# Kernel tuning notes

Measured on AMD Instinct MI355X. Metric: run time of the kernel, lower is better.

Reference implementation:

```python
import jax, jax.numpy as jnp
import numpy as np

H = 8       # num_heads
HD = 32     # transformer_head_dim
LN_EPS = 1e-5


def _layernorm(x, g, b):
    m = jnp.mean(x, axis=-1, keepdims=True)
    v = jnp.mean(jnp.square(x - m), axis=-1, keepdims=True)
    return (x - m) * jax.lax.rsqrt(v + LN_EPS) * g + b


def setup_inputs() -> dict:
    key = jax.random.key(0)
    ks = jax.random.split(key, 8)
    D, DFF = 256, 1024
    B, N = 8, 2048
    s = 0.02  # weight init scale
    return {
        "x": jax.random.normal(ks[0], (B, N, D), jnp.float32),
        "w_qkv": jax.random.normal(ks[1], (3 * H * HD, D), jnp.float32) * s,
        "w_out": jax.random.normal(ks[2], (D, H * HD), jnp.float32) * s,
        "b_out": jnp.zeros((D,), jnp.float32),
        "w1": jax.random.normal(ks[3], (DFF, D), jnp.float32) * s,
        "wv": jax.random.normal(ks[4], (DFF, D), jnp.float32) * s,
        "w2": jax.random.normal(ks[5], (D, DFF), jnp.float32) * s,
        "ln1_g": jnp.ones((D,), jnp.float32),
        "ln1_b": jnp.zeros((D,), jnp.float32),
        "ln2_g": jnp.ones((D,), jnp.float32),
        "ln2_b": jnp.zeros((D,), jnp.float32),
    }


def reference(x, w_qkv, w_out, b_out, w1, wv, w2, ln1_g, ln1_b, ln2_g, ln2_b):
    B, N, D = x.shape
    scale = HD ** (-0.5)
    # --- MultiHeadedAttention ---
    qkv = x @ w_qkv.T                                   # [B,N,3*H*HD]
    q, k, v = jnp.split(qkv, 3, axis=-1)
    def to_heads(t):
        return t.reshape(B, N, H, HD).transpose(0, 2, 1, 3)  # [B,H,N,HD]
    q, k, v = to_heads(q), to_heads(k), to_heads(v)
    sim = jnp.einsum("bhid,bhjd->bhij", q, k) * scale   # [B,H,N,N]
    attn = jax.nn.softmax(sim, axis=-1)
    o = jnp.einsum("bhij,bhjd->bhid", attn, v)
    o = o.transpose(0, 2, 1, 3).reshape(B, N, H * HD)
    y = o @ w_out.T + b_out                             # attn output
    # --- attn AddNorm: ln(dropout(y)+x), dropout off ---
    x1 = _layernorm(y + x, ln1_g, ln1_b)
    # --- GEGLU FFN applied to y (faithful to source) ---
    ff = jax.nn.gelu(y @ w1.T, approximate=False) * (y @ wv.T)
    ff = ff @ w2.T
    # --- ff AddNorm ---
    return _layernorm(ff + x1, ln2_g, ln2_b)
```

## Files before the change

### kernel.cpp

```cpp
#include <hip/hip_runtime.h>

typedef unsigned short u16;
typedef __bf16 bf16;
typedef __bf16 bf16x8 __attribute__((ext_vector_type(8)));
typedef float f32x4 __attribute__((ext_vector_type(4)));
typedef unsigned short u16x8 __attribute__((ext_vector_type(8)));
typedef unsigned short u16x4 __attribute__((ext_vector_type(4)));
typedef unsigned short u16x2 __attribute__((ext_vector_type(2)));

#define DEVI static __device__ __forceinline__

DEVI float bf2f(u16 h) { return __builtin_bit_cast(float, (unsigned)h << 16); }
DEVI u16 cvt_bf(float f) { return __builtin_bit_cast(u16, (bf16)f); }

DEVI void gload16(const u16* g, u16* l) {
  __builtin_amdgcn_global_load_lds(
      (const __attribute__((address_space(1))) void*)g,
      (__attribute__((address_space(3))) void*)l, 16, 0, 0);
}

DEVI float gelu_exact(float x) {
  return 0.5f * x * (1.0f + erff(x * 0.70710678118654752f));
}

__global__ __launch_bounds__(256) void k_cast(const float* __restrict__ x,
                                              const float* __restrict__ wqkv,
                                              const float* __restrict__ wout,
                                              const float* __restrict__ w1,
                                              const float* __restrict__ wv,
                                              const float* __restrict__ w2,
                                              u16* __restrict__ dst0) {
  long i = (long)blockIdx.x * 256 + threadIdx.x;
  const float* src;
  u16* dst;
  long off;
  if (i < 1048576)       { src = x;    dst = dst0;           off = i; }
  else if (i < 1097728)  { src = wqkv; dst = dst0 + 4194304; off = i - 1048576; }
  else if (i < 1114112)  { src = wout; dst = dst0 + 4390912; off = i - 1097728; }
  else if (i < 1179648)  { src = w1;   dst = dst0 + 4456448; off = i - 1114112; }
  else if (i < 1245184)  { src = wv;   dst = dst0 + 4718592; off = i - 1179648; }
  else                   { src = w2;   dst = dst0 + 4980736; off = i - 1245184; }
  float4 f = reinterpret_cast<const float4*>(src)[off];
  u16x4 o;
  o[0] = cvt_bf(f.x); o[1] = cvt_bf(f.y); o[2] = cvt_bf(f.z); o[3] = cvt_bf(f.w);
  reinterpret_cast<u16x4*>(dst)[off] = o;
}

template <int BM, int BN, int NI>
__global__ __launch_bounds__(256) void k_gemm(const u16* __restrict__ A, const u16* __restrict__ B0,
                                              const u16* __restrict__ B1, int Nsplit,
                                              const float* __restrict__ bias,
                                              u16* __restrict__ C, int N, int K) {
  constexpr int MI = BM / 32;
  __shared__ u16 Alds[BM * 64];
  __shared__ u16 Blds[BN * 64];
  const int m0 = blockIdx.x * BM;
  const int n0 = blockIdx.y * BN;
  const u16* Ap = A + (long)m0 * K;
  const u16* Bp = (n0 < Nsplit) ? (B0 + (long)n0 * K) : (B1 + (long)(n0 - Nsplit) * K);
  const int tid = threadIdx.x, lane = tid & 63, wave = tid >> 6;
  const int wr = (wave >> 1) * (BM / 2), wc = (wave & 1) * (BN / 2);
  const int lr = lane & 15, g = lane >> 4;
  const int sr = lane >> 3, sg = lane & 7;

  f32x4 acc[MI][NI] = {};
  const int nk = K >> 6;
  for (int kt = 0; kt < nk; ++kt) {
    const int kb = kt << 6;
    __syncthreads();
#pragma unroll
    for (int c = 0; c < BM / 32; ++c) {
      const int row = wave * (BM / 4) + c * 8 + sr;
      gload16(Ap + (long)row * K + kb + ((sg ^ (row & 7)) << 3),
              &Alds[(wave * (BM / 4) + c * 8) << 6]);
    }
#pragma unroll
    for (int c = 0; c < BN / 32; ++c) {
      const int row = wave * (BN / 4) + c * 8 + sr;
      gload16(Bp + (long)row * K + kb + ((sg ^ ((row / NI) & 7)) << 3),
              &Blds[(wave * (BN / 4) + c * 8) << 6]);
    }
    __syncthreads();
#pragma unroll
    for (int kk = 0; kk < 2; ++kk) {
      bf16x8 av[MI], bv[NI];
#pragma unroll
      for (int i = 0; i < MI; ++i) {
        const int ra = wr + i * 16 + lr;
        av[i] = *reinterpret_cast<const bf16x8*>(&Alds[(ra << 6) + (((kk * 4 + g) ^ (ra & 7)) << 3)]);
      }
#pragma unroll
      for (int ni = 0; ni < NI; ++ni) {
        const int rb = wc + lr * NI + ni;
        bv[ni] = *reinterpret_cast<const bf16x8*>(&Blds[(rb << 6) + (((kk * 4 + g) ^ ((rb / NI) & 7)) << 3)]);
      }
#pragma unroll
      for (int mi = 0; mi < MI; ++mi)
#pragma unroll
        for (int ni = 0; ni < NI; ++ni)
          acc[mi][ni] = __builtin_amdgcn_mfma_f32_16x16x32_bf16(av[mi], bv[ni], acc[mi][ni], 0, 0, 0);
    }
  }
  const int colb = n0 + wc + lr * NI;
  float bvv[NI];
#pragma unroll
  for (int ni = 0; ni < NI; ++ni) bvv[ni] = bias ? bias[colb + ni] : 0.0f;
#pragma unroll
  for (int mi = 0; mi < MI; ++mi) {
#pragma unroll
    for (int r = 0; r < 4; ++r) {
      const long row = m0 + wr + mi * 16 + g * 4 + r;
      if constexpr (NI == 4) {
        u16x4 v;
#pragma unroll
        for (int ni = 0; ni < 4; ++ni) v[ni] = cvt_bf(acc[mi][ni][r] + bvv[ni]);
        *reinterpret_cast<u16x4*>(C + row * N + colb) = v;
      } else {
        u16x2 v;
#pragma unroll
        for (int ni = 0; ni < 2; ++ni) v[ni] = cvt_bf(acc[mi][ni][r] + bvv[ni]);
        *reinterpret_cast<u16x2*>(C + row * N + colb) = v;
      }
    }
  }
}

__global__ __launch_bounds__(256) void k_glu(const u16* __restrict__ A, const u16* __restrict__ W1,
                                             const u16* __restrict__ Wv, u16* __restrict__ C) {
  constexpr int K = 256, N = 1024;
  __shared__ u16 Alds[128 * 64];
  __shared__ u16 Blds[64 * 64];
  const int m0 = blockIdx.x * 128;
  const int n0h = blockIdx.y * 32;
  const u16* Ap = A + (long)m0 * K;
  const int tid = threadIdx.x, lane = tid & 63, wave = tid >> 6;
  const int lr = lane & 15, g = lane >> 4;
  const int sr = lane >> 3, sg = lane & 7;

  f32x4 acc[2][4] = {};
  for (int kt = 0; kt < 4; ++kt) {
    const int kb = kt << 6;
    __syncthreads();
#pragma unroll
    for (int c = 0; c < 4; ++c) {
      const int row = wave * 32 + c * 8 + sr;
      gload16(Ap + (long)row * K + kb + ((sg ^ (row & 7)) << 3), &Alds[(wave * 32 + c * 8) << 6]);
    }
#pragma unroll
    for (int c = 0; c < 2; ++c) {
      const int row = wave * 16 + c * 8 + sr;
      const u16* bp = (row & 1) ? Wv : W1;
      gload16(bp + (long)(n0h + (row >> 1)) * K + kb + ((sg ^ ((row >> 2) & 7)) << 3),
              &Blds[(wave * 16 + c * 8) << 6]);
    }
    __syncthreads();
#pragma unroll
    for (int kk = 0; kk < 2; ++kk) {
      bf16x8 av[2], bv[4];
#pragma unroll
      for (int i = 0; i < 2; ++i) {
        const int ra = wave * 32 + i * 16 + lr;
        av[i] = *reinterpret_cast<const bf16x8*>(&Alds[(ra << 6) + (((kk * 4 + g) ^ (ra & 7)) << 3)]);
      }
#pragma unroll
      for (int ni = 0; ni < 4; ++ni) {
        const int rb = lr * 4 + ni;
        bv[ni] = *reinterpret_cast<const bf16x8*>(&Blds[(rb << 6) + (((kk * 4 + g) ^ ((rb >> 2) & 7)) << 3)]);
      }
#pragma unroll
      for (int mi = 0; mi < 2; ++mi)
#pragma unroll
        for (int ni = 0; ni < 4; ++ni)
          acc[mi][ni] = __builtin_amdgcn_mfma_f32_16x16x32_bf16(av[mi], bv[ni], acc[mi][ni], 0, 0, 0);
    }
  }
  const int j0 = n0h + lr * 2;
#pragma unroll
  for (int mi = 0; mi < 2; ++mi) {
#pragma unroll
    for (int r = 0; r < 4; ++r) {
      const long row = m0 + wave * 32 + mi * 16 + g * 4 + r;
      u16x2 v;
      v[0] = cvt_bf(gelu_exact(acc[mi][0][r]) * acc[mi][1][r]);
      v[1] = cvt_bf(gelu_exact(acc[mi][2][r]) * acc[mi][3][r]);
      *reinterpret_cast<u16x2*>(C + row * N + j0) = v;
    }
  }
}

__global__ __launch_bounds__(256) void k_vt(const u16* __restrict__ qkv, u16* __restrict__ vt) {
  const int bh = blockIdx.x & 63, nt = blockIdx.x >> 6;
  const int b = bh >> 3, h = bh & 7;
  const int wave = threadIdx.x >> 6, lane = threadIdx.x & 63;
  const int dcol = wave * 8;
#pragma unroll
  for (int i = 0; i < 4; ++i) {
    const int nn = nt * 256 + i * 64 + lane;
    u16x8 v = *reinterpret_cast<const u16x8*>(qkv + (long)(b * 2048 + nn) * 768 + 512 + h * 32 + dcol);
#pragma unroll
    for (int j = 0; j < 8; ++j)
      vt[(long)(bh * 32 + dcol + j) * 2048 + nn] = v[j];
  }
}

__global__ __launch_bounds__(512) void k_attn(const u16* __restrict__ qkv, const u16* __restrict__ vt,
                                              u16* __restrict__ o) {
  __shared__ u16 Klds[2 * 4096];
  __shared__ u16 Vlds[2 * 4096];
  __shared__ u16 Plds[8 * 1024];
  const int id = blockIdx.x;
  const int qt = id >> 6, bh = id & 63;
  const int b = bh >> 3, h = bh & 7;
  const int tid = threadIdx.x, wave = tid >> 6, lane = tid & 63;
  const int lq = lane & 15, g = lane >> 4, lqh = lq & 7;

  const long qrow = (long)(b * 2048 + qt * 128 + wave * 16 + lq);
  u16x8 qraw = *reinterpret_cast<const u16x8*>(qkv + qrow * 768 + h * 32 + g * 8);
  bf16x8 qf;
#pragma unroll
  for (int j = 0; j < 8; ++j) qf[j] = (bf16)(bf2f(qraw[j]) * 0.25503486f);

  const int rK = tid >> 3, gpK = tid & 7, lK = gpK ^ (rK & 7);
  const u16* ksrc = qkv + (long)(b * 2048 + (lK >> 2) * 64 + rK) * 768 + 256 + h * 32 + (lK & 3) * 8;
  const int dV = tid >> 4, gpV = tid & 15, lV = (gpV & 8) | ((gpV & 7) ^ (dV & 7));
  const u16* vsrc = vt + (long)(bh * 32 + dV) * 2048 + lV * 8;
  u16* kdst = Klds + wave * 512;
  u16* vdst = Vlds + wave * 512;

  gload16(ksrc, kdst);
  gload16(vsrc, vdst);

  float m = -1e30f, l = 0.0f;
  f32x4 oacc[2] = {};
  const f32x4 zero = {0.0f, 0.0f, 0.0f, 0.0f};
  u16* Pw = Plds + wave * 1024;

  for (int kt = 0; kt < 16; ++kt) {
    const int bo = (kt & 1) * 4096;
    __syncthreads();
    if (kt + 1 < 16) {
      const int nbo = ((kt + 1) & 1) * 4096;
      gload16(ksrc + (long)(kt + 1) * 98304, kdst + nbo);
      gload16(vsrc + (kt + 1) * 128, vdst + nbo);
    }
    f32x4 s[8];
#pragma unroll
    for (int f = 0; f < 8; ++f) {
      const bf16x8 kf = *reinterpret_cast<const bf16x8*>(
          &Klds[bo + (((f & 3) * 16 + lq) << 6) + ((((f >> 2) * 4 + g) ^ lqh) << 3)]);
      s[f] = __builtin_amdgcn_mfma_f32_16x16x32_bf16(kf, qf, zero, 0, 0, 0);
    }
    float tmax = -1e30f;
#pragma unroll
    for (int f = 0; f < 8; ++f)
#pragma unroll
      for (int r = 0; r < 4; ++r) tmax = fmaxf(tmax, s[f][r]);
    tmax = fmaxf(tmax, __shfl_xor(tmax, 16));
    tmax = fmaxf(tmax, __shfl_xor(tmax, 32));
    const float mnew = fmaxf(m, tmax);
    const float alpha = exp2f(m - mnew);
    float rsum = 0.0f;
#pragma unroll
    for (int f = 0; f < 8; ++f)
#pragma unroll
      for (int r = 0; r < 4; ++r) {
        const float p = exp2f(s[f][r] - mnew);
        s[f][r] = p;
        rsum += p;
      }
    rsum += __shfl_xor(rsum, 16);
    rsum += __shfl_xor(rsum, 32);
    l = l * alpha + rsum;
    m = mnew;
#pragma unroll
    for (int di = 0; di < 2; ++di)
#pragma unroll
      for (int r = 0; r < 4; ++r) oacc[di][r] *= alpha;

#pragma unroll
    for (int pass = 0; pass < 2; ++pass) {
#pragma unroll
      for (int fi = 0; fi < 4; ++fi) {
        const int f = pass * 4 + fi;
        u16x4 pk;
#pragma unroll
        for (int r = 0; r < 4; ++r) pk[r] = cvt_bf(s[f][r]);
        *reinterpret_cast<u16x4*>(
            &Pw[(lq << 6) + (((fi * 2 + (g >> 1)) ^ lqh) << 3) + ((g & 1) << 2)]) = pk;
      }
#pragma unroll
      for (int ks2 = 0; ks2 < 2; ++ks2) {
        const bf16x8 pf = *reinterpret_cast<const bf16x8*>(
            &Pw[(lq << 6) + (((ks2 * 4 + g) ^ lqh) << 3)]);
        const int gl = (pass * 2 + ks2) * 4 + g;
        const int gp = (gl & 8) | ((gl & 7) ^ lqh);
#pragma unroll
        for (int di = 0; di < 2; ++di) {
          const bf16x8 vf = *reinterpret_cast<const bf16x8*>(
              &Vlds[bo + (((di * 16 + lq)) << 7) + (gp << 3)]);
          oacc[di] = __builtin_amdgcn_mfma_f32_16x16x32_bf16(vf, pf, oacc[di], 0, 0, 0);
        }
      }
    }
  }

  const float inv = 1.0f / l;
  const long orow = (long)(b * 2048 + qt * 128 + wave * 16 + lq);
#pragma unroll
  for (int di = 0; di < 2; ++di) {
    u16x4 ov;
#pragma unroll
    for (int r = 0; r < 4; ++r) ov[r] = cvt_bf(oacc[di][r] * inv);
    *reinterpret_cast<u16x4*>(o + orow * 256 + h * 32 + di * 16 + g * 4) = ov;
  }
}

__global__ __launch_bounds__(256) void k_ln(const u16* __restrict__ yin, const float* __restrict__ xres,
                                            const float* __restrict__ gw, const float* __restrict__ bw,
                                            float* __restrict__ out) {
  const int row = blockIdx.x * 4 + (threadIdx.x >> 6);
  const int lane = threadIdx.x & 63;
  const long base = (long)row * 256 + lane * 4;
  const float4 xv = *reinterpret_cast<const float4*>(xres + base);
  const u16x4 yv = *reinterpret_cast<const u16x4*>(yin + base);
  float s0 = bf2f(yv[0]) + xv.x;
  float s1 = bf2f(yv[1]) + xv.y;
  float s2 = bf2f(yv[2]) + xv.z;
  float s3 = bf2f(yv[3]) + xv.w;
  float sum = s0 + s1 + s2 + s3;
  float sq = s0 * s0 + s1 * s1 + s2 * s2 + s3 * s3;
#pragma unroll
  for (int msk = 1; msk < 64; msk <<= 1) {
    sum += __shfl_xor(sum, msk);
    sq += __shfl_xor(sq, msk);
  }
  const float mean = sum * (1.0f / 256.0f);
  const float var = sq * (1.0f / 256.0f) - mean * mean;
  const float rstd = rsqrtf(var + 1e-5f);
  const int c = lane * 4;
  float4 ov;
  ov.x = (s0 - mean) * rstd * gw[c + 0] + bw[c + 0];
  ov.y = (s1 - mean) * rstd * gw[c + 1] + bw[c + 1];
  ov.z = (s2 - mean) * rstd * gw[c + 2] + bw[c + 2];
  ov.w = (s3 - mean) * rstd * gw[c + 3] + bw[c + 3];
  *reinterpret_cast<float4*>(out + base) = ov;
}

extern "C" void kernel_launch(void* const* d_in, const int* in_sizes, int n_in,
                              void* d_out, int out_size, void* d_ws, size_t ws_size,
                              hipStream_t stream) {
  (void)in_sizes; (void)n_in; (void)out_size;
  if (ws_size < 136314880ULL) return;

  const float* x     = (const float*)d_in[0];
  const float* w_qkv = (const float*)d_in[1];
  const float* w_out = (const float*)d_in[2];
  const float* b_out = (const float*)d_in[3];
  const float* w1    = (const float*)d_in[4];
  const float* wv    = (const float*)d_in[5];
  const float* w2    = (const float*)d_in[6];
  const float* ln1g  = (const float*)d_in[7];
  const float* ln1b  = (const float*)d_in[8];
  const float* ln2g  = (const float*)d_in[9];
  const float* ln2b  = (const float*)d_in[10];
  float* outp = (float*)d_out;

  char* ws = (char*)d_ws;
  u16* xb    = (u16*)ws;
  u16* wqkvb = xb + 4194304;
  u16* woutb = wqkvb + 196608;
  u16* w1b   = woutb + 65536;
  u16* wvb   = w1b + 262144;
  u16* w2b   = wvb + 262144;
  u16* qkvb  = w2b + 262144;
  u16* ob    = qkvb + 12582912;
  u16* yb    = ob + 4194304;
  float* x1  = (float*)(ws + 52428800);
  u16* vtb   = (u16*)(ws + 69206016);
  u16* ffin  = qkvb;
  u16* ff2   = xb;

  k_cast<<<5120, 256, 0, stream>>>(x, w_qkv, w_out, w1, wv, w2, xb);
  k_gemm<128, 128, 4><<<dim3(128, 6), 256, 0, stream>>>(xb, wqkvb, wqkvb, 1 << 30, nullptr, qkvb, 768, 256);
  k_vt<<<512, 256, 0, stream>>>(qkvb, vtb);
  k_attn<<<1024, 512, 0, stream>>>(qkvb, vtb, ob);
  k_gemm<128, 64, 2><<<dim3(128, 4), 256, 0, stream>>>(ob, woutb, woutb, 1 << 30, b_out, yb, 256, 256);
  k_ln<<<4096, 256, 0, stream>>>(yb, x, ln1g, ln1b, x1);
  k_glu<<<dim3(128, 32), 256, 0, stream>>>(yb, w1b, wvb, ffin);
  k_gemm<128, 64, 2><<<dim3(128, 4), 256, 0, stream>>>(ffin, w2b, w2b, 1 << 30, nullptr, ff2, 256, 1024);
  k_ln<<<4096, 256, 0, stream>>>(ff2, x1, ln2g, ln2b, outp);
}
```

Measured before the change: 269.7 us.

## Feed softmax probabilities to PV MFMA from registers, skip LDS round-trip

The attention kernel no longer writes the bf16 probability tile to LDS and reads it back. The S accumulator layout is fed straight into 16x16x16 MFMAs, and the V LDS swizzle is changed to match that layout. The row sum is computed with an MFMA against a ones vector, and the running-max rescale is skipped unless some lane's max grows by more than 8 (lazy rescaling). The cost is twice as many smaller MFMAs and slightly looser numerics from the deferred max update.

```diff
diff --git a/kernel.cpp b/kernel.cpp
--- a/kernel.cpp
+++ b/kernel.cpp
@@ -3,6 +3,8 @@
 typedef unsigned short u16;
 typedef __bf16 bf16;
 typedef __bf16 bf16x8 __attribute__((ext_vector_type(8)));
+typedef __bf16 bf16x4 __attribute__((ext_vector_type(4)));
+typedef short s16x4 __attribute__((ext_vector_type(4)));
 typedef float f32x4 __attribute__((ext_vector_type(4)));
 typedef unsigned short u16x8 __attribute__((ext_vector_type(8)));
 typedef unsigned short u16x4 __attribute__((ext_vector_type(4)));
@@ -21,6 +23,18 @@
 
 DEVI float gelu_exact(float x) {
   return 0.5f * x * (1.0f + erff(x * 0.70710678118654752f));
+}
+
+DEVI f32x4 mfma16(bf16x4 a, bf16x4 b, f32x4 c) {
+#if __has_builtin(__builtin_amdgcn_mfma_f32_16x16x16bf16_1k)
+  return __builtin_amdgcn_mfma_f32_16x16x16bf16_1k(
+      __builtin_bit_cast(s16x4, a), __builtin_bit_cast(s16x4, b), c, 0, 0, 0);
+#else
+  f32x4 r = c;
+  asm volatile("s_nop 1\n\tv_mfma_f32_16x16x16_bf16 %0, %1, %2, %0\n\ts_nop 7\n\ts_nop 3"
+               : "+v"(r) : "v"(a), "v"(b));
+  return r;
+#endif
 }
 
 __global__ __launch_bounds__(256) void k_cast(const float* __restrict__ x,
@@ -207,7 +221,6 @@
                                               u16* __restrict__ o) {
   __shared__ u16 Klds[2 * 4096];
   __shared__ u16 Vlds[2 * 4096];
-  __shared__ u16 Plds[8 * 1024];
   const int id = blockIdx.x;
   const int qt = id >> 6, bh = id & 63;
   const int b = bh >> 3, h = bh & 7;
@@ -222,18 +235,20 @@
 
   const int rK = tid >> 3, gpK = tid & 7, lK = gpK ^ (rK & 7);
   const u16* ksrc = qkv + (long)(b * 2048 + (lK >> 2) * 64 + rK) * 768 + 256 + h * 32 + (lK & 3) * 8;
-  const int dV = tid >> 4, gpV = tid & 15, lV = (gpV & 8) | ((gpV & 7) ^ (dV & 7));
-  const u16* vsrc = vt + (long)(bh * 32 + dV) * 2048 + lV * 8;
+  const int dV = tid >> 4, gpV = tid & 15, lgV = gpV ^ ((dV & 3) << 1);
+  const u16* vsrc = vt + (long)(bh * 32 + dV) * 2048 + lgV * 8;
   u16* kdst = Klds + wave * 512;
   u16* vdst = Vlds + wave * 512;
 
   gload16(ksrc, kdst);
   gload16(vsrc, vdst);
 
-  float m = -1e30f, l = 0.0f;
+  float m = -1e30f;
   f32x4 oacc[2] = {};
+  f32x4 lacc = {};
   const f32x4 zero = {0.0f, 0.0f, 0.0f, 0.0f};
-  u16* Pw = Plds + wave * 1024;
+  bf16x4 onesf;
+  onesf[0] = onesf[1] = onesf[2] = onesf[3] = (bf16)1.0f;
 
   for (int kt = 0; kt < 16; ++kt) {
     const int bo = (kt & 1) * 4096;
@@ -252,59 +267,47 @@
     }
     float tmax = -1e30f;
 #pragma unroll
+    for (int f = 0; f < 8; ++f) {
+      const float m01 = fmaxf(s[f][0], s[f][1]);
+      const float m23 = fmaxf(s[f][2], s[f][3]);
+      tmax = fmaxf(tmax, fmaxf(m01, m23));
+    }
+    if (__any(tmax > m + 8.0f)) {
+      tmax = fmaxf(tmax, __shfl_xor(tmax, 16));
+      tmax = fmaxf(tmax, __shfl_xor(tmax, 32));
+      const float mnew = fmaxf(m, tmax);
+      const float alpha = exp2f(m - mnew);
+#pragma unroll
+      for (int di = 0; di < 2; ++di)
+#pragma unroll
+        for (int r = 0; r < 4; ++r) oacc[di][r] *= alpha;
+#pragma unroll
+      for (int r = 0; r < 4; ++r) lacc[r] *= alpha;
+      m = mnew;
+    }
+#pragma unroll
     for (int f = 0; f < 8; ++f)
 #pragma unroll
-      for (int r = 0; r < 4; ++r) tmax = fmaxf(tmax, s[f][r]);
-    tmax = fmaxf(tmax, __shfl_xor(tmax, 16));
-    tmax = fmaxf(tmax, __shfl_xor(tmax, 32));
-    const float mnew = fmaxf(m, tmax);
-    const float alpha = exp2f(m - mnew);
-    float rsum = 0.0f;
-#pragma unroll
-    for (int f = 0; f < 8; ++f)
-#pragma unroll
-      for (int r = 0; r < 4; ++r) {
-        const float p = exp2f(s[f][r] - mnew);
-        s[f][r] = p;
-        rsum += p;
-      }
-    rsum += __shfl_xor(rsum, 16);
-    rsum += __shfl_xor(rsum, 32);
-    l = l * alpha + rsum;
-    m = mnew;
-#pragma unroll
-    for (int di = 0; di < 2; ++di)
-#pragma unroll
-      for (int r = 0; r < 4; ++r) oacc[di][r] *= alpha;
-
-#pragma unroll
-    for (int pass = 0; pass < 2; ++pass) {
-#pragma unroll
-      for (int fi = 0; fi < 4; ++fi) {
-        const int f = pass * 4 + fi;
-        u16x4 pk;
-#pragma unroll
-        for (int r = 0; r < 4; ++r) pk[r] = cvt_bf(s[f][r]);
-        *reinterpret_cast<u16x4*>(
-            &Pw[(lq << 6) + (((fi * 2 + (g >> 1)) ^ lqh) << 3) + ((g & 1) << 2)]) = pk;
-      }
-#pragma unroll
-      for (int ks2 = 0; ks2 < 2; ++ks2) {
-        const bf16x8 pf = *reinterpret_cast<const bf16x8*>(
-            &Pw[(lq << 6) + (((ks2 * 4 + g) ^ lqh) << 3)]);
-        const int gl = (pass * 2 + ks2) * 4 + g;
-        const int gp = (gl & 8) | ((gl & 7) ^ lqh);
-#pragma unroll
-        for (int di = 0; di < 2; ++di) {
-          const bf16x8 vf = *reinterpret_cast<const bf16x8*>(
-              &Vlds[bo + (((di * 16 + lq)) << 7) + (gp << 3)]);
-          oacc[di] = __builtin_amdgcn_mfma_f32_16x16x32_bf16(vf, pf, oacc[di], 0, 0, 0);
-        }
-      }
-    }
-  }
-
-  const float inv = 1.0f / l;
+      for (int r = 0; r < 4; ++r) s[f][r] = exp2f(s[f][r] - m);
+
+#pragma unroll
+    for (int f = 0; f < 8; ++f) {
+      bf16x4 pf4;
+      pf4[0] = (bf16)s[f][0]; pf4[1] = (bf16)s[f][1];
+      pf4[2] = (bf16)s[f][2]; pf4[3] = (bf16)s[f][3];
+      lacc = mfma16(onesf, pf4, lacc);
+      const int gl8 = (f >> 2) * 16 + (f & 3) * 4 + g;
+      const int ph8 = gl8 ^ ((lq & 3) << 2);
+#pragma unroll
+      for (int di = 0; di < 2; ++di) {
+        const int d = di * 16 + lq;
+        const bf16x4 vf = *reinterpret_cast<const bf16x4*>(&Vlds[bo + d * 128 + ph8 * 4]);
+        oacc[di] = mfma16(vf, pf4, oacc[di]);
+      }
+    }
+  }
+
+  const float inv = 1.0f / lacc[0];
   const long orow = (long)(b * 2048 + qt * 128 + wave * 16 + lq);
 #pragma unroll
   for (int di = 0; di < 2; ++di) {
```

Result: slower. 276.5 us (+2.5%).
